# Kernel optimization log

Measured on AMD Instinct MI355X. Metric: run time of the kernel, lower is better.

## Reference

```python
import jax, jax.numpy as jnp
import numpy as np

B, GRID, DM, DEPTH = 4, 12, 384, 8
L = GRID ** 3                      # 1728 tokens
DI, NS, DC, DTR = 768, 16, 4, 24   # d_inner, d_state, d_conv, dt_rank
KEEP = 432


def _sincos_pos_embed(grid, dim):
    g = np.arange(grid, dtype=np.float32)
    gh, gw, gd = np.meshgrid(g, g, g, indexing='ij')
    pd = dim // 6
    omega = 1.0 / (10000.0 ** (np.arange(pd, dtype=np.float32) / pd))
    parts = []
    for v in (gh, gw, gd):
        o = np.einsum('m,d->md', v.reshape(-1), omega)
        parts += [np.sin(o), np.cos(o)]
    return np.concatenate(parts, axis=1)[None].astype(np.float32)  # (1, L, dim)


def setup_inputs():
    key = jax.random.key(0)
    ks = jax.random.split(key, 16)
    n = lambda k, s, sc=0.02: jax.random.normal(k, s, jnp.float32) * sc
    # mamba dt_proj bias init: inverse softplus of dt ~ LogUniform(1e-3, 1e-1)
    dt = jnp.exp(jax.random.uniform(ks[9], (DEPTH, DI)) * (np.log(0.1) - np.log(0.001)) + np.log(0.001))
    dt_proj_b = dt + jnp.log(-jnp.expm1(-dt))
    A_log = jnp.log(jnp.broadcast_to(jnp.arange(1, NS + 1, dtype=jnp.float32), (DEPTH, DI, NS)))
    rng = np.random.default_rng(0)
    act = np.zeros((B, L), np.int32)
    for b in range(B):
        act[b, rng.permutation(L)[:KEEP]] = 1
    return {
        'imgs': n(ks[0], (B, DM, GRID, GRID, GRID), 1.0),
        'pos_embed': jnp.asarray(_sincos_pos_embed(GRID, DM)),
        'mask_token': n(ks[1], (DM,)),
        'norm1_w': jnp.ones((DEPTH, DM)), 'norm1_b': jnp.zeros((DEPTH, DM)),
        'in_proj_w': n(ks[2], (DEPTH, 2 * DI, DM)),
        'conv_w': n(ks[3], (DEPTH, DI, DC), 0.1), 'conv_b': jnp.zeros((DEPTH, DI)),
        'x_proj_w': n(ks[4], (DEPTH, DTR + 2 * NS, DI)),
        'dt_proj_w': n(ks[5], (DEPTH, DI, DTR), 0.1), 'dt_proj_b': dt_proj_b,
        'A_log': A_log, 'A_b_log': A_log,
        'D_skip': jnp.ones((DEPTH, DI)),
        'out_proj_w': n(ks[6], (DEPTH, DM, DI)),
        'norm2_w': jnp.ones((DEPTH, DM)), 'norm2_b': jnp.zeros((DEPTH, DM)),
        'fc1_w': n(ks[7], (DEPTH, 2 * DM, DM)), 'fc1_b': jnp.zeros((DEPTH, 2 * DM)),
        'fc2_w': n(ks[8], (DEPTH, DM, 2 * DM)), 'fc2_b': jnp.zeros((DEPTH, DM)),
        'active': jnp.asarray(act.reshape(B, 1, GRID, GRID, GRID)),
        'len_keep': KEEP,
    }


def _ln(x, w, b):
    mu = jnp.mean(x, -1, keepdims=True)
    v = jnp.var(x, -1, keepdims=True)
    return (x - mu) * jax.lax.rsqrt(v + 1e-5) * w + b


def _ssm_dir(xr, z, conv_w, conv_b, xpw, dtw, dtb, a_log, dskip):
    # xr, z: (B, DI, Lk) pre-conv streams; causal depthwise conv then selective scan
    Lk = xr.shape[-1]
    xp = jnp.pad(xr, ((0, 0), (0, 0), (DC - 1, 0)))
    x = sum(conv_w[:, k][None, :, None] * xp[:, :, k:k + Lk] for k in range(DC))
    x = jax.nn.silu(x + conv_b[None, :, None])
    xdb = jnp.einsum('bdl,rd->brl', x, xpw)
    dtr, Bm, Cm = xdb[:, :DTR], xdb[:, DTR:DTR + NS], xdb[:, DTR + NS:]
    delta = jax.nn.softplus(jnp.einsum('brl,dr->bdl', dtr, dtw) + dtb[None, :, None])
    A = -jnp.exp(a_log)                              # (DI, NS)
    dl = delta.transpose(0, 2, 1)                    # (B, Lk, DI)
    xt = x.transpose(0, 2, 1)                        # (B, Lk, DI)
    dA = jnp.exp(dl[..., None] * A)                  # (B, Lk, DI, NS)
    dBx = dl[..., None] * Bm.transpose(0, 2, 1)[:, :, None, :] * xt[..., None]
    Ct = Cm.transpose(0, 2, 1)                       # (B, Lk, NS)

    def step(h, inp):
        a, bx, c = inp
        h = a * h + bx
        return h, jnp.einsum('bdn,bn->bd', h, c)

    h0 = jnp.zeros((xr.shape[0], DI, NS), xr.dtype)
    _, ys = jax.lax.scan(step, h0, (dA.transpose(1, 0, 2, 3), dBx.transpose(1, 0, 2, 3), Ct.transpose(1, 0, 2)))
    y = ys.transpose(1, 0, 2) + dskip * xt           # (B, Lk, DI)
    return y * jax.nn.silu(z.transpose(0, 2, 1))


def _block(x, p):
    (n1w, n1b, inW, cw, cb, xpw, dtw, dtb, al, abl, dsk, ow, n2w, n2b, f1w, f1b, f2w, f2b) = p
    h = _ln(x, n1w, n1b)
    xz = h @ inW.T                                   # (B, Lk, 2*DI)
    xr = xz[..., :DI].transpose(0, 2, 1)
    z = xz[..., DI:].transpose(0, 2, 1)
    yf = _ssm_dir(xr, z, cw, cb, xpw, dtw, dtb, al, dsk)
    yb = _ssm_dir(xr[:, :, ::-1], z[:, :, ::-1], cw, cb, xpw, dtw, dtb, abl, dsk)[:, ::-1]
    x = x + (yf + yb) @ ow.T
    h2 = _ln(x, n2w, n2b)
    return x + (jax.nn.gelu(h2 @ f1w.T + f1b, approximate=False) @ f2w.T + f2b)


def _forward(imgs, pos_embed, mask_token, norm1_w, norm1_b, in_proj_w, conv_w, conv_b,
             x_proj_w, dt_proj_w, dt_proj_b, A_log, A_b_log, D_skip, out_proj_w,
             norm2_w, norm2_b, fc1_w, fc1_b, fc2_w, fc2_b, active, len_keep):
    x = imgs.reshape(B, DM, L).transpose(0, 2, 1) + pos_embed   # (B, L, DM)
    mask = active.reshape(B, L).astype(jnp.int32)               # (B, L) 1=keep
    ids_shuffle = jnp.argsort(1 - mask, axis=1)                 # kept tokens first
    ids_restore = jnp.argsort(ids_shuffle, axis=1)
    ids_keep = ids_shuffle[:, :len_keep]
    xk = jnp.take_along_axis(x, jnp.broadcast_to(ids_keep[:, :, None], (B, len_keep, DM)), axis=1)
    blk = jax.checkpoint(_block)
    for i in range(DEPTH):
        p = (norm1_w[i], norm1_b[i], in_proj_w[i], conv_w[i], conv_b[i], x_proj_w[i],
             dt_proj_w[i], dt_proj_b[i], A_log[i], A_b_log[i], D_skip[i], out_proj_w[i],
             norm2_w[i], norm2_b[i], fc1_w[i], fc1_b[i], fc2_w[i], fc2_b[i])
        xk = blk(xk, p)
    mt = jnp.broadcast_to(mask_token, (B, L - len_keep, DM))
    x_ = jnp.concatenate([xk, mt], axis=1)
    x = jnp.take_along_axis(x_, jnp.broadcast_to(ids_restore[:, :, None], (B, L, DM)), axis=1)
    return x.transpose(0, 2, 1).reshape(B, DM, GRID, GRID, GRID)


def reference(imgs, pos_embed, mask_token, norm1_w, norm1_b, in_proj_w, conv_w, conv_b,
              x_proj_w, dt_proj_w, dt_proj_b, A_log, A_b_log, D_skip, out_proj_w,
              norm2_w, norm2_b, fc1_w, fc1_b, fc2_w, fc2_b, active, len_keep):
    return _forward(imgs, pos_embed, mask_token, norm1_w, norm1_b, in_proj_w, conv_w, conv_b,
                    x_proj_w, dt_proj_w, dt_proj_b, A_log, A_b_log, D_skip, out_proj_w,
                    norm2_w, norm2_b, fc1_w, fc1_b, fc2_w, fc2_b, active, len_keep)
```

## Files before the change

### kernel.cpp

```cpp
#include <hip/hip_runtime.h>
#include <hip/hip_bf16.h>
#include <math.h>

#define B_    4
#define GRID_ 12
#define DM_   384
#define DEPTH_ 8
#define L_    1728
#define DI_   768
#define NS_   16
#define DC_   4
#define DTR_  24
#define KEEP_ 432
#define XPR_  56
#define NC_   16
#define CL_   27
#define XSPLIT_ 4

typedef __attribute__((ext_vector_type(8))) short short8;
typedef __attribute__((ext_vector_type(4))) float floatx4;

__device__ __forceinline__ float silu_f(float x) {
    return x / (1.0f + __expf(-x));
}
__device__ __forceinline__ float softplus_f(float x) {
    return (x > 20.0f) ? x : log1pf(expf(x));
}
__device__ __forceinline__ float gelu_exact_f(float x) {
    return 0.5f * x * (1.0f + erff(x * 0.7071067811865476f));
}
__device__ __forceinline__ unsigned short f2bf(float x) {
    union { float f; unsigned int u; } c; c.f = x;
    unsigned int u = c.u;
    unsigned int r = (u + 0x7fffu + ((u >> 16) & 1u)) >> 16;
    return (unsigned short)r;
}

#define S0_ (DEPTH_ * 2 * DI_ * DM_)
#define S1_ (DEPTH_ * XPR_ * DI_)
#define S2_ (DEPTH_ * DI_ * DTR_)
#define S3_ (DEPTH_ * DM_ * DI_)
#define S4_ (DEPTH_ * 2 * DM_ * DM_)
#define S5_ (DEPTH_ * DM_ * 2 * DM_)
#define WTOT_ (S0_ + S1_ + S2_ + S3_ + S4_ + S5_)

__global__ void cast_weights_k(const float* __restrict__ w0,
                               const float* __restrict__ w1,
                               const float* __restrict__ w2,
                               const float* __restrict__ w3,
                               const float* __restrict__ w4,
                               const float* __restrict__ w5,
                               unsigned short* __restrict__ out) {
    int i = blockIdx.x * 256 + threadIdx.x;
    if (i >= WTOT_) return;
    float v;
    if (i < S0_) v = w0[i];
    else if (i < S0_ + S1_) v = w1[i - S0_];
    else if (i < S0_ + S1_ + S2_) v = w2[i - S0_ - S1_];
    else if (i < S0_ + S1_ + S2_ + S3_) v = w3[i - S0_ - S1_ - S2_];
    else if (i < S0_ + S1_ + S2_ + S3_ + S4_) v = w4[i - S0_ - S1_ - S2_ - S3_];
    else v = w5[i - S0_ - S1_ - S2_ - S3_ - S4_];
    out[i] = f2bf(v);
}

__global__ __launch_bounds__(256) void compute_ids_k(
        const int* __restrict__ active,
        int* __restrict__ RANK, int* __restrict__ IDS) {
    __shared__ int cnt[256];
    int b = blockIdx.x;
    int t = threadIdx.x;
    const int PER = (L_ + 255) / 256;
    int base = t * PER;
    int c = 0;
    for (int j = 0; j < PER; ++j) {
        int l = base + j;
        if (l < L_ && active[b * L_ + l]) ++c;
    }
    cnt[t] = c;
    __syncthreads();
    for (int off = 1; off < 256; off <<= 1) {
        int v = (t >= off) ? cnt[t - off] : 0;
        __syncthreads();
        cnt[t] += v;
        __syncthreads();
    }
    int r = cnt[t] - c;
    for (int j = 0; j < PER; ++j) {
        int l = base + j;
        if (l >= L_) break;
        if (active[b * L_ + l]) {
            RANK[b * L_ + l] = r;
            IDS[b * KEEP_ + r] = l;
            ++r;
        } else {
            RANK[b * L_ + l] = -1;
        }
    }
}

__global__ void gather_embed_k(const float* __restrict__ imgs,
                               const float* __restrict__ pos,
                               const int* __restrict__ IDS,
                               float* __restrict__ X) {
    int tid = blockIdx.x * 256 + threadIdx.x;
    if (tid >= B_ * KEEP_ * DM_) return;
    int c = tid % DM_;
    int i = (tid / DM_) % KEEP_;
    int b = tid / (DM_ * KEEP_);
    int l = IDS[b * KEEP_ + i];
    X[tid] = imgs[((size_t)b * DM_ + c) * L_ + l] + pos[(size_t)l * DM_ + c];
}

__global__ void final_scatter_k(const float* __restrict__ X,
                                const float* __restrict__ mask_token,
                                const int* __restrict__ RANK,
                                float* __restrict__ out) {
    int tid = blockIdx.x * 256 + threadIdx.x;
    if (tid >= B_ * DM_ * L_) return;
    int l = tid % L_;
    int c = (tid / L_) % DM_;
    int b = tid / (L_ * DM_);
    int r = RANK[b * L_ + l];
    out[tid] = (r >= 0) ? X[((size_t)b * KEEP_ + r) * DM_ + c] : mask_token[c];
}

__global__ void layernorm_k(const float* __restrict__ X,
                            const float* __restrict__ w,
                            const float* __restrict__ bia,
                            float* __restrict__ H, int rows) {
    int row = blockIdx.x * 4 + (threadIdx.x >> 6);
    int lane = threadIdx.x & 63;
    if (row >= rows) return;
    const float* x = X + (size_t)row * DM_;
    float v[6];
    float s = 0.0f;
#pragma unroll
    for (int j = 0; j < 6; ++j) { v[j] = x[lane + 64 * j]; s += v[j]; }
#pragma unroll
    for (int m = 1; m < 64; m <<= 1) s += __shfl_xor(s, m);
    float mu = s * (1.0f / DM_);
    float s2 = 0.0f;
#pragma unroll
    for (int j = 0; j < 6; ++j) { float d = v[j] - mu; s2 += d * d; }
#pragma unroll
    for (int m = 1; m < 64; m <<= 1) s2 += __shfl_xor(s2, m);
    float rs = rsqrtf(s2 * (1.0f / DM_) + 1e-5f);
    float* h = H + (size_t)row * DM_;
#pragma unroll
    for (int j = 0; j < 6; ++j) {
        int c = lane + 64 * j;
        h[c] = (v[j] - mu) * rs * w[c] + bia[c];
    }
}

__global__ __launch_bounds__(256) void gemm_mfma_k(
    const float* __restrict__ A, const float* __restrict__ A2, int lda,
    int aslabs, size_t aslabstride,
    const unsigned short* __restrict__ Wb,
    const float* __restrict__ bias,
    float* __restrict__ C, int ldc,
    int M, int N, int K, int kslices, int mode) {
    __shared__ unsigned short As[2][64][32];
    __shared__ unsigned short Bs[2][64][32];
    int t = threadIdx.x;
    int wave = t >> 6;
    int lane = t & 63;
    int q = lane >> 4;
    int ml = lane & 15;
    int m0 = blockIdx.y * 64;
    int n0 = blockIdx.x * 64;
    int z  = blockIdx.z;
    int Kper = K / kslices;
    int kbeg = z * Kper;
    int kend = kbeg + Kper;
    if (mode == 8) C += (size_t)z * M * ldc;

    int srow = t >> 2;
    int scol = (t & 3) * 8;

    const bool nfull = (N - n0) >= 64;

    floatx4 acc[4];
#pragma unroll
    for (int i = 0; i < 4; ++i) acc[i] = (floatx4){0.f, 0.f, 0.f, 0.f};

    float ra[8];
    uint4 rb;

    auto loadA = [&](int k0) {
        if (k0 + 32 <= kend) {
            const float* ap = A + (size_t)(m0 + srow) * lda + k0 + scol;
            floatx4 v0 = *(const floatx4*)ap;
            floatx4 v1 = *(const floatx4*)(ap + 4);
            for (int sl = 1; sl < aslabs; ++sl) {
                const float* ap2 = ap + sl * aslabstride;
                v0 += *(const floatx4*)ap2;
                v1 += *(const floatx4*)(ap2 + 4);
            }
            if (A2) {
                const float* ap2 = A2 + (size_t)(m0 + srow) * lda + k0 + scol;
                v0 += *(const floatx4*)ap2;
                v1 += *(const floatx4*)(ap2 + 4);
            }
#pragma unroll
            for (int j = 0; j < 4; ++j) { ra[j] = v0[j]; ra[4 + j] = v1[j]; }
        } else {
#pragma unroll
            for (int j = 0; j < 8; ++j) {
                int kk = k0 + scol + j;
                float v = 0.0f;
                if (kk < kend) {
                    size_t ai = (size_t)(m0 + srow) * lda + kk;
                    v = A[ai];
                    for (int sl = 1; sl < aslabs; ++sl) v += A[ai + sl * aslabstride];
                    if (A2) v += A2[ai];
                }
                ra[j] = v;
            }
        }
    };
    auto loadB = [&](int k0) {
        if (nfull && (k0 + 32 <= kend)) {
            rb = *(const uint4*)(Wb + (size_t)(n0 + srow) * K + k0 + scol);
        } else {
            unsigned short tmp[8];
#pragma unroll
            for (int j = 0; j < 8; ++j) {
                int kk = k0 + scol + j;
                unsigned short v = 0;
                if ((n0 + srow) < N && kk < kend)
                    v = Wb[(size_t)(n0 + srow) * K + kk];
                tmp[j] = v;
            }
            rb = *(const uint4*)tmp;
        }
    };
    auto storeT = [&](int buf) {
#pragma unroll
        for (int j = 0; j < 8; ++j) As[buf][srow][scol + j] = f2bf(ra[j]);
        *(uint4*)&Bs[buf][srow][scol] = rb;
    };

    int nk = (Kper + 31) >> 5;
    loadA(kbeg);
    loadB(kbeg);
    storeT(0);
    __syncthreads();
    int buf = 0;
    for (int it = 0; it < nk; ++it) {
        if (it + 1 < nk) {
            int kn = kbeg + (it + 1) * 32;
            loadA(kn);
            loadB(kn);
        }
        short8 a = *(const short8*)&As[buf][wave * 16 + ml][q * 8];
#pragma unroll
        for (int ns = 0; ns < 4; ++ns) {
            short8 b = *(const short8*)&Bs[buf][ns * 16 + ml][q * 8];
            acc[ns] = __builtin_amdgcn_mfma_f32_16x16x32_bf16(a, b, acc[ns], 0, 0, 0);
        }
        if (it + 1 < nk) {
            storeT(buf ^ 1);
            __syncthreads();
            buf ^= 1;
        }
    }

#pragma unroll
    for (int ns = 0; ns < 4; ++ns) {
        int n = n0 + ns * 16 + ml;
        if (n >= N) continue;
#pragma unroll
        for (int r = 0; r < 4; ++r) {
            int m = m0 + wave * 16 + q * 4 + r;
            float v = acc[ns][r];
            size_t ci = (size_t)m * ldc + n;
            if (mode == 2) {
                C[ci] = softplus_f(v + bias[n]);
            } else if (mode == 3) {
                C[ci] = gelu_exact_f(v + bias[n]);
            } else if (mode == 4) {
                C[ci] = v + C[ci];
            } else if (mode == 5) {
                C[ci] = v + C[ci] + bias[n];
            } else if (mode == 6) {
                atomicAdd(&C[ci], v);
            } else if (mode == 7) {
                if (z == 0) v += bias[n];
                atomicAdd(&C[ci], v);
            } else {
                C[ci] = v;
            }
        }
    }
}

__global__ void conv_silu_k(const float* __restrict__ XZ,
                            const float* __restrict__ cw,
                            const float* __restrict__ cb,
                            float* __restrict__ XCONV) {
    int tid = blockIdx.x * 256 + threadIdx.x;
    if (tid >= 2 * B_ * KEEP_ * DI_) return;
    int d = tid % DI_;
    int s = (tid / DI_) % KEEP_;
    int b = (tid / (DI_ * KEEP_)) % B_;
    int dir = tid / (DI_ * KEEP_ * B_);
    float v = cb[d];
#pragma unroll
    for (int k = 0; k < DC_; ++k) {
        int j = s - (DC_ - 1) + k;
        if (j >= 0) {
            int la = dir ? (KEEP_ - 1 - j) : j;
            v += cw[d * DC_ + k] * XZ[((size_t)b * KEEP_ + la) * (2 * DI_) + d];
        }
    }
    XCONV[tid] = silu_f(v);
}

#define PSL_ ((size_t)(2 * B_ * KEEP_) * XPR_)

__global__ __launch_bounds__(256) void scan_partial_k(
        const float* __restrict__ DELTA,
        const float* __restrict__ XCONV,
        const float* __restrict__ PART,
        const float* __restrict__ Alog,
        const float* __restrict__ Ablog,
        float* __restrict__ HFIN,
        float* __restrict__ SDELT) {
    __shared__ float sB[CL_][NS_];
    int blk = blockIdx.x;
    int g   = blk % 3;
    int c   = (blk / 3) % NC_;
    int b   = (blk / (3 * NC_)) % B_;
    int dir = blk / (3 * NC_ * B_);
    int t = threadIdx.x;
    int d = g * 256 + t;
    size_t base = (size_t)(dir * B_ + b) * KEEP_ + c * CL_;

    for (int i = t; i < CL_ * NS_; i += 256) {
        int s = i >> 4, n = i & 15;
        size_t idx = (base + s) * XPR_ + DTR_ + n;
        float v = PART[idx];
#pragma unroll
        for (int sl = 1; sl < XSPLIT_; ++sl) v += PART[idx + sl * PSL_];
        sB[s][n] = v;
    }
    __syncthreads();

    const float* alog = dir ? Ablog : Alog;
    float Av[NS_];
#pragma unroll
    for (int n = 0; n < NS_; ++n) Av[n] = -__expf(alog[d * NS_ + n]);
    float h[NS_];
#pragma unroll
    for (int n = 0; n < NS_; ++n) h[n] = 0.0f;
    float sdel = 0.0f;

    float nd = DELTA[base * DI_ + d];
    float nx = XCONV[base * DI_ + d];
    for (int s = 0; s < CL_; ++s) {
        float delta = nd, xv = nx;
        if (s + 1 < CL_) {
            nd = DELTA[(base + s + 1) * DI_ + d];
            nx = XCONV[(base + s + 1) * DI_ + d];
        }
        sdel += delta;
        float dx = delta * xv;
#pragma unroll
        for (int n = 0; n < NS_; ++n)
            h[n] = __expf(delta * Av[n]) * h[n] + dx * sB[s][n];
    }
    size_t o = ((size_t)(dir * B_ + b) * NC_ + c) * DI_ + d;
    SDELT[o] = sdel;
#pragma unroll
    for (int n = 0; n < NS_; ++n) HFIN[o * NS_ + n] = h[n];
}

__global__ __launch_bounds__(256) void scan_combine_k(
        const float* __restrict__ HFIN,
        const float* __restrict__ SDELT,
        const float* __restrict__ Alog,
        const float* __restrict__ Ablog,
        float* __restrict__ HINIT) {
    int gid = blockIdx.x * 256 + threadIdx.x;
    int n = gid & 15;
    int d = (gid >> 4) % DI_;
    int b = (gid / (16 * DI_)) % B_;
    int dir = gid / (16 * DI_ * B_);
    const float* alog = dir ? Ablog : Alog;
    float Av = -__expf(alog[d * NS_ + n]);
    float hi = 0.0f;
#pragma unroll
    for (int c = 0; c < NC_; ++c) {
        size_t o = ((size_t)(dir * B_ + b) * NC_ + c) * DI_ + d;
        HINIT[o * NS_ + n] = hi;
        hi = __expf(Av * SDELT[o]) * hi + HFIN[o * NS_ + n];
    }
}

__global__ __launch_bounds__(256) void scan_final_k(
        const float* __restrict__ DELTA,
        const float* __restrict__ XCONV,
        const float* __restrict__ PART,
        const float* __restrict__ XZ,
        const float* __restrict__ Alog,
        const float* __restrict__ Ablog,
        const float* __restrict__ dskip,
        const float* __restrict__ HINIT,
        float* __restrict__ YOUT) {
    __shared__ float sB[CL_][NS_];
    __shared__ float sC[CL_][NS_];
    int blk = blockIdx.x;
    int g   = blk % 3;
    int c   = (blk / 3) % NC_;
    int b   = (blk / (3 * NC_)) % B_;
    int dir = blk / (3 * NC_ * B_);
    int t = threadIdx.x;
    int d = g * 256 + t;
    size_t base = (size_t)(dir * B_ + b) * KEEP_ + c * CL_;

    for (int i = t; i < CL_ * NS_; i += 256) {
        int s = i >> 4, n = i & 15;
        size_t ib = (base + s) * XPR_ + DTR_ + n;
        size_t ic = ib + NS_;
        float vb = PART[ib], vc = PART[ic];
#pragma unroll
        for (int sl = 1; sl < XSPLIT_; ++sl) {
            vb += PART[ib + sl * PSL_];
            vc += PART[ic + sl * PSL_];
        }
        sB[s][n] = vb;
        sC[s][n] = vc;
    }
    __syncthreads();

    const float* alog = dir ? Ablog : Alog;
    float Av[NS_];
#pragma unroll
    for (int n = 0; n < NS_; ++n) Av[n] = -__expf(alog[d * NS_ + n]);
    float dsk = dskip[d];
    size_t o = ((size_t)(dir * B_ + b) * NC_ + c) * DI_ + d;
    float h[NS_];
#pragma unroll
    for (int n = 0; n < NS_; ++n) h[n] = HINIT[o * NS_ + n];

    float nd = DELTA[base * DI_ + d];
    float nx = XCONV[base * DI_ + d];
    for (int s = 0; s < CL_; ++s) {
        float delta = nd, xv = nx;
        if (s + 1 < CL_) {
            nd = DELTA[(base + s + 1) * DI_ + d];
            nx = XCONV[(base + s + 1) * DI_ + d];
        }
        float dx = delta * xv;
        float y = 0.0f;
#pragma unroll
        for (int n = 0; n < NS_; ++n) {
            h[n] = __expf(delta * Av[n]) * h[n] + dx * sB[s][n];
            y += h[n] * sC[s][n];
        }
        int pos = c * CL_ + s;
        int la = dir ? (KEEP_ - 1 - pos) : pos;
        float z = XZ[((size_t)b * KEEP_ + la) * (2 * DI_) + DI_ + d];
        YOUT[((size_t)(dir * B_ + b) * KEEP_ + la) * DI_ + d] =
            (y + dsk * xv) * silu_f(z);
    }
}

extern "C" void kernel_launch(void* const* d_in, const int* in_sizes, int n_in,
                              void* d_out, int out_size, void* d_ws, size_t ws_size,
                              hipStream_t stream) {
    const float* imgs      = (const float*)d_in[0];
    const float* pos       = (const float*)d_in[1];
    const float* mask_tok  = (const float*)d_in[2];
    const float* n1w       = (const float*)d_in[3];
    const float* n1b       = (const float*)d_in[4];
    const float* inW       = (const float*)d_in[5];
    const float* cw        = (const float*)d_in[6];
    const float* cb        = (const float*)d_in[7];
    const float* xpw       = (const float*)d_in[8];
    const float* dtw       = (const float*)d_in[9];
    const float* dtb       = (const float*)d_in[10];
    const float* Alog      = (const float*)d_in[11];
    const float* Ablog     = (const float*)d_in[12];
    const float* dskip     = (const float*)d_in[13];
    const float* ow        = (const float*)d_in[14];
    const float* n2w       = (const float*)d_in[15];
    const float* n2b       = (const float*)d_in[16];
    const float* f1w       = (const float*)d_in[17];
    const float* f1b       = (const float*)d_in[18];
    const float* f2w       = (const float*)d_in[19];
    const float* f2b       = (const float*)d_in[20];
    const int*   active    = (const int*)d_in[21];
    float* out = (float*)d_out;

    char* w = (char*)d_ws;
    auto alloc = [&](size_t bytes) {
        void* p = (void*)w;
        w += (bytes + 255) & ~(size_t)255;
        return p;
    };
    int*   RANK  = (int*)  alloc((size_t)B_ * L_ * 4);
    int*   IDS   = (int*)  alloc((size_t)B_ * KEEP_ * 4);
    float* X     = (float*)alloc((size_t)B_ * KEEP_ * DM_ * 4);
    float* H     = (float*)alloc((size_t)B_ * KEEP_ * DM_ * 4);
    float* XZ    = (float*)alloc((size_t)B_ * KEEP_ * 2 * DI_ * 4);
    float* XCONV = (float*)alloc((size_t)2 * B_ * KEEP_ * DI_ * 4);
    float* PART  = (float*)alloc((size_t)XSPLIT_ * 2 * B_ * KEEP_ * XPR_ * 4);
    float* DELTA = (float*)alloc((size_t)2 * B_ * KEEP_ * DI_ * 4);
    float* YOUT  = (float*)alloc((size_t)2 * B_ * KEEP_ * DI_ * 4);
    float* G     = (float*)alloc((size_t)B_ * KEEP_ * DI_ * 4);
    float* HFIN  = (float*)alloc((size_t)2 * B_ * NC_ * DI_ * NS_ * 4);
    float* HINIT = (float*)alloc((size_t)2 * B_ * NC_ * DI_ * NS_ * 4);
    float* SDELT = (float*)alloc((size_t)2 * B_ * NC_ * DI_ * 4);
    unsigned short* WB = (unsigned short*)alloc((size_t)WTOT_ * 2);

    const unsigned short* wInB = WB;
    const unsigned short* wXpB = WB + S0_;
    const unsigned short* wDtB = WB + S0_ + S1_;
    const unsigned short* wOwB = WB + S0_ + S1_ + S2_;
    const unsigned short* wF1B = WB + S0_ + S1_ + S2_ + S3_;
    const unsigned short* wF2B = WB + S0_ + S1_ + S2_ + S3_ + S4_;

    const int ROWS = B_ * KEEP_;
    const int ROWS2 = 2 * B_ * KEEP_;
    const int SCAN_BLOCKS = 2 * B_ * NC_ * 3;
    const size_t PSLAB = (size_t)ROWS2 * XPR_;

    cast_weights_k<<<(WTOT_ + 255) / 256, 256, 0, stream>>>(
        inW, xpw, dtw, ow, f1w, f2w, (unsigned short*)WB);
    compute_ids_k<<<B_, 256, 0, stream>>>(active, RANK, IDS);
    gather_embed_k<<<(B_ * KEEP_ * DM_ + 255) / 256, 256, 0, stream>>>(imgs, pos, IDS, X);

    for (int layer = 0; layer < DEPTH_; ++layer) {
        const unsigned short* L_inW = wInB + (size_t)layer * 2 * DI_ * DM_;
        const float* L_cw  = cw  + (size_t)layer * DI_ * DC_;
        const float* L_cb  = cb  + (size_t)layer * DI_;
        const unsigned short* L_xpw = wXpB + (size_t)layer * XPR_ * DI_;
        const unsigned short* L_dtw = wDtB + (size_t)layer * DI_ * DTR_;
        const float* L_dtb = dtb + (size_t)layer * DI_;
        const float* L_Al  = Alog  + (size_t)layer * DI_ * NS_;
        const float* L_Abl = Ablog + (size_t)layer * DI_ * NS_;
        const float* L_dsk = dskip + (size_t)layer * DI_;
        const unsigned short* L_ow  = wOwB + (size_t)layer * DM_ * DI_;
        const unsigned short* L_f1w = wF1B + (size_t)layer * 2 * DM_ * DM_;
        const float* L_f1b = f1b + (size_t)layer * 2 * DM_;
        const unsigned short* L_f2w = wF2B + (size_t)layer * DM_ * 2 * DM_;
        const float* L_f2b = f2b + (size_t)layer * DM_;

        layernorm_k<<<(ROWS + 3) / 4, 256, 0, stream>>>(
            X, n1w + layer * DM_, n1b + layer * DM_, H, ROWS);
        gemm_mfma_k<<<dim3((2 * DI_) / 64, ROWS / 64), 256, 0, stream>>>(
            H, nullptr, DM_, 1, 0, L_inW, nullptr, XZ, 2 * DI_,
            ROWS, 2 * DI_, DM_, 1, 0);
        conv_silu_k<<<(2 * B_ * KEEP_ * DI_ + 255) / 256, 256, 0, stream>>>(
            XZ, L_cw, L_cb, XCONV);
        gemm_mfma_k<<<dim3(1, ROWS2 / 64, XSPLIT_), 256, 0, stream>>>(
            XCONV, nullptr, DI_, 1, 0, L_xpw, nullptr, PART, XPR_,
            ROWS2, XPR_, DI_, XSPLIT_, 8);
        gemm_mfma_k<<<dim3(DI_ / 64, ROWS2 / 64), 256, 0, stream>>>(
            PART, nullptr, XPR_, XSPLIT_, PSLAB, L_dtw, L_dtb, DELTA, DI_,
            ROWS2, DI_, DTR_, 1, 2);
        scan_partial_k<<<SCAN_BLOCKS, 256, 0, stream>>>(
            DELTA, XCONV, PART, L_Al, L_Abl, HFIN, SDELT);
        scan_combine_k<<<(2 * B_ * DI_ * NS_) / 256, 256, 0, stream>>>(
            HFIN, SDELT, L_Al, L_Abl, HINIT);
        scan_final_k<<<SCAN_BLOCKS, 256, 0, stream>>>(
            DELTA, XCONV, PART, XZ, L_Al, L_Abl, L_dsk, HINIT, YOUT);
        gemm_mfma_k<<<dim3(DM_ / 64, ROWS / 64, 2), 256, 0, stream>>>(
            YOUT, YOUT + (size_t)B_ * KEEP_ * DI_, DI_, 1, 0, L_ow, nullptr,
            X, DM_, ROWS, DM_, DI_, 2, 6);
        layernorm_k<<<(ROWS + 3) / 4, 256, 0, stream>>>(
            X, n2w + layer * DM_, n2b + layer * DM_, H, ROWS);
        gemm_mfma_k<<<dim3((2 * DM_) / 64, ROWS / 64), 256, 0, stream>>>(
            H, nullptr, DM_, 1, 0, L_f1w, L_f1b, G, 2 * DM_,
            ROWS, 2 * DM_, DM_, 1, 3);
        gemm_mfma_k<<<dim3(DM_ / 64, ROWS / 64, 2), 256, 0, stream>>>(
            G, nullptr, 2 * DM_, 1, 0, L_f2w, L_f2b, X, DM_,
            ROWS, DM_, 2 * DM_, 2, 7);
    }

    final_scatter_k<<<(B_ * DM_ * L_ + 255) / 256, 256, 0, stream>>>(
        X, mask_tok, RANK, out);
}
```

Before: 1.522 ms.

## Fuse conv+dt_proj into scan and x_proj, emit bf16 activations

Fuses the depthwise conv+SiLU into the x_proj GEMM's A-load and recomputes conv and the dt_proj+softplus inside both scan kernels from XZ and the x_proj partials. This removes the XCONV and DELTA intermediates and two kernel launches per layer. LayerNorm and the fc1 GELU epilogue now write bf16, so the GEMMs load bf16 A directly. LDS tiles are padded to cut bank conflicts and the bounds-check paths are dropped. In exchange the conv and dt work is computed twice (once per scan pass), and the scan kernels use more shared memory, which may lower occupancy.

```diff
diff --git a/kernel.cpp b/kernel.cpp
--- a/kernel.cpp
+++ b/kernel.cpp
@@ -38,15 +38,13 @@
 
 #define S0_ (DEPTH_ * 2 * DI_ * DM_)
 #define S1_ (DEPTH_ * XPR_ * DI_)
-#define S2_ (DEPTH_ * DI_ * DTR_)
 #define S3_ (DEPTH_ * DM_ * DI_)
 #define S4_ (DEPTH_ * 2 * DM_ * DM_)
 #define S5_ (DEPTH_ * DM_ * 2 * DM_)
-#define WTOT_ (S0_ + S1_ + S2_ + S3_ + S4_ + S5_)
+#define WTOT_ (S0_ + S1_ + S3_ + S4_ + S5_)
 
 __global__ void cast_weights_k(const float* __restrict__ w0,
                                const float* __restrict__ w1,
-                               const float* __restrict__ w2,
                                const float* __restrict__ w3,
                                const float* __restrict__ w4,
                                const float* __restrict__ w5,
@@ -56,10 +54,9 @@
     float v;
     if (i < S0_) v = w0[i];
     else if (i < S0_ + S1_) v = w1[i - S0_];
-    else if (i < S0_ + S1_ + S2_) v = w2[i - S0_ - S1_];
-    else if (i < S0_ + S1_ + S2_ + S3_) v = w3[i - S0_ - S1_ - S2_];
-    else if (i < S0_ + S1_ + S2_ + S3_ + S4_) v = w4[i - S0_ - S1_ - S2_ - S3_];
-    else v = w5[i - S0_ - S1_ - S2_ - S3_ - S4_];
+    else if (i < S0_ + S1_ + S3_) v = w3[i - S0_ - S1_];
+    else if (i < S0_ + S1_ + S3_ + S4_) v = w4[i - S0_ - S1_ - S3_];
+    else v = w5[i - S0_ - S1_ - S3_ - S4_];
     out[i] = f2bf(v);
 }
 
@@ -127,7 +124,7 @@
 __global__ void layernorm_k(const float* __restrict__ X,
                             const float* __restrict__ w,
                             const float* __restrict__ bia,
-                            float* __restrict__ H, int rows) {
+                            unsigned short* __restrict__ H, int rows) {
     int row = blockIdx.x * 4 + (threadIdx.x >> 6);
     int lane = threadIdx.x & 63;
     if (row >= rows) return;
@@ -145,23 +142,24 @@
 #pragma unroll
     for (int m = 1; m < 64; m <<= 1) s2 += __shfl_xor(s2, m);
     float rs = rsqrtf(s2 * (1.0f / DM_) + 1e-5f);
-    float* h = H + (size_t)row * DM_;
+    unsigned short* h = H + (size_t)row * DM_;
 #pragma unroll
     for (int j = 0; j < 6; ++j) {
         int c = lane + 64 * j;
-        h[c] = (v[j] - mu) * rs * w[c] + bia[c];
-    }
-}
-
+        h[c] = f2bf((v[j] - mu) * rs * w[c] + bia[c]);
+    }
+}
+
+#define APAD_ 40
 __global__ __launch_bounds__(256) void gemm_mfma_k(
-    const float* __restrict__ A, const float* __restrict__ A2, int lda,
-    int aslabs, size_t aslabstride,
+    const void* __restrict__ Ap, const float* __restrict__ A2, int lda,
+    int abf16,
     const unsigned short* __restrict__ Wb,
     const float* __restrict__ bias,
     float* __restrict__ C, int ldc,
     int M, int N, int K, int kslices, int mode) {
-    __shared__ unsigned short As[2][64][32];
-    __shared__ unsigned short Bs[2][64][32];
+    __shared__ unsigned short As[2][64][APAD_];
+    __shared__ unsigned short Bs[2][64][APAD_];
     int t = threadIdx.x;
     int wave = t >> 6;
     int lane = t & 63;
@@ -172,31 +170,25 @@
     int z  = blockIdx.z;
     int Kper = K / kslices;
     int kbeg = z * Kper;
-    int kend = kbeg + Kper;
-    if (mode == 8) C += (size_t)z * M * ldc;
 
     int srow = t >> 2;
     int scol = (t & 3) * 8;
 
-    const bool nfull = (N - n0) >= 64;
-
     floatx4 acc[4];
 #pragma unroll
     for (int i = 0; i < 4; ++i) acc[i] = (floatx4){0.f, 0.f, 0.f, 0.f};
 
     float ra[8];
-    uint4 rb;
+    uint4 rau, rb;
 
     auto loadA = [&](int k0) {
-        if (k0 + 32 <= kend) {
-            const float* ap = A + (size_t)(m0 + srow) * lda + k0 + scol;
+        if (abf16) {
+            rau = *(const uint4*)((const unsigned short*)Ap +
+                                  (size_t)(m0 + srow) * lda + k0 + scol);
+        } else {
+            const float* ap = (const float*)Ap + (size_t)(m0 + srow) * lda + k0 + scol;
             floatx4 v0 = *(const floatx4*)ap;
             floatx4 v1 = *(const floatx4*)(ap + 4);
-            for (int sl = 1; sl < aslabs; ++sl) {
-                const float* ap2 = ap + sl * aslabstride;
-                v0 += *(const floatx4*)ap2;
-                v1 += *(const floatx4*)(ap2 + 4);
-            }
             if (A2) {
                 const float* ap2 = A2 + (size_t)(m0 + srow) * lda + k0 + scol;
                 v0 += *(const floatx4*)ap2;
@@ -204,44 +196,22 @@
             }
 #pragma unroll
             for (int j = 0; j < 4; ++j) { ra[j] = v0[j]; ra[4 + j] = v1[j]; }
-        } else {
-#pragma unroll
-            for (int j = 0; j < 8; ++j) {
-                int kk = k0 + scol + j;
-                float v = 0.0f;
-                if (kk < kend) {
-                    size_t ai = (size_t)(m0 + srow) * lda + kk;
-                    v = A[ai];
-                    for (int sl = 1; sl < aslabs; ++sl) v += A[ai + sl * aslabstride];
-                    if (A2) v += A2[ai];
-                }
-                ra[j] = v;
-            }
         }
     };
     auto loadB = [&](int k0) {
-        if (nfull && (k0 + 32 <= kend)) {
-            rb = *(const uint4*)(Wb + (size_t)(n0 + srow) * K + k0 + scol);
-        } else {
-            unsigned short tmp[8];
-#pragma unroll
-            for (int j = 0; j < 8; ++j) {
-                int kk = k0 + scol + j;
-                unsigned short v = 0;
-                if ((n0 + srow) < N && kk < kend)
-                    v = Wb[(size_t)(n0 + srow) * K + kk];
-                tmp[j] = v;
-            }
-            rb = *(const uint4*)tmp;
-        }
+        rb = *(const uint4*)(Wb + (size_t)(n0 + srow) * K + k0 + scol);
     };
     auto storeT = [&](int buf) {
-#pragma unroll
-        for (int j = 0; j < 8; ++j) As[buf][srow][scol + j] = f2bf(ra[j]);
+        if (abf16) {
+            *(uint4*)&As[buf][srow][scol] = rau;
+        } else {
+#pragma unroll
+            for (int j = 0; j < 8; ++j) As[buf][srow][scol + j] = f2bf(ra[j]);
+        }
         *(uint4*)&Bs[buf][srow][scol] = rb;
     };
 
-    int nk = (Kper + 31) >> 5;
+    int nk = Kper >> 5;
     loadA(kbeg);
     loadB(kbeg);
     storeT(0);
@@ -269,25 +239,18 @@
 #pragma unroll
     for (int ns = 0; ns < 4; ++ns) {
         int n = n0 + ns * 16 + ml;
-        if (n >= N) continue;
 #pragma unroll
         for (int r = 0; r < 4; ++r) {
             int m = m0 + wave * 16 + q * 4 + r;
             float v = acc[ns][r];
             size_t ci = (size_t)m * ldc + n;
-            if (mode == 2) {
-                C[ci] = softplus_f(v + bias[n]);
-            } else if (mode == 3) {
-                C[ci] = gelu_exact_f(v + bias[n]);
-            } else if (mode == 4) {
-                C[ci] = v + C[ci];
-            } else if (mode == 5) {
-                C[ci] = v + C[ci] + bias[n];
-            } else if (mode == 6) {
+            if (mode == 6) {
                 atomicAdd(&C[ci], v);
             } else if (mode == 7) {
                 if (z == 0) v += bias[n];
                 atomicAdd(&C[ci], v);
+            } else if (mode == 9) {
+                ((unsigned short*)C)[ci] = f2bf(gelu_exact_f(v + bias[n]));
             } else {
                 C[ci] = v;
             }
@@ -295,39 +258,137 @@
     }
 }
 
-__global__ void conv_silu_k(const float* __restrict__ XZ,
-                            const float* __restrict__ cw,
-                            const float* __restrict__ cb,
-                            float* __restrict__ XCONV) {
-    int tid = blockIdx.x * 256 + threadIdx.x;
-    if (tid >= 2 * B_ * KEEP_ * DI_) return;
-    int d = tid % DI_;
-    int s = (tid / DI_) % KEEP_;
-    int b = (tid / (DI_ * KEEP_)) % B_;
-    int dir = tid / (DI_ * KEEP_ * B_);
-    float v = cb[d];
-#pragma unroll
-    for (int k = 0; k < DC_; ++k) {
-        int j = s - (DC_ - 1) + k;
-        if (j >= 0) {
-            int la = dir ? (KEEP_ - 1 - j) : j;
-            v += cw[d * DC_ + k] * XZ[((size_t)b * KEEP_ + la) * (2 * DI_) + d];
-        }
-    }
-    XCONV[tid] = silu_f(v);
+__global__ __launch_bounds__(256) void xproj_conv_k(
+        const float* __restrict__ XZ,
+        const float* __restrict__ cw,
+        const float* __restrict__ cb,
+        const unsigned short* __restrict__ Wb,
+        float* __restrict__ Cout) {
+    __shared__ unsigned short As[2][64][APAD_];
+    __shared__ unsigned short Bs[2][64][APAD_];
+    int t = threadIdx.x;
+    int wave = t >> 6;
+    int lane = t & 63;
+    int q = lane >> 4;
+    int ml = lane & 15;
+    int m0 = blockIdx.y * 64;
+    int z  = blockIdx.z;
+    const int Kper = DI_ / XSPLIT_;
+    int kbeg = z * Kper;
+    float* C = Cout + (size_t)z * (2 * B_ * KEEP_) * XPR_;
+
+    int srow = t >> 2;
+    int scol = (t & 3) * 8;
+    int m = m0 + srow;
+    int dir = m / (B_ * KEEP_);
+    int rem = m - dir * (B_ * KEEP_);
+    int b = rem / KEEP_;
+    int s = rem - b * KEEP_;
+
+    floatx4 acc[4];
+#pragma unroll
+    for (int i = 0; i < 4; ++i) acc[i] = (floatx4){0.f, 0.f, 0.f, 0.f};
+
+    float ra[8];
+    uint4 rb;
+
+    auto loadA = [&](int k0) {
+        int d0 = k0 + scol;
+        float v[8];
+        {
+            floatx4 c0v = *(const floatx4*)(cb + d0);
+            floatx4 c1v = *(const floatx4*)(cb + d0 + 4);
+#pragma unroll
+            for (int j = 0; j < 4; ++j) { v[j] = c0v[j]; v[4 + j] = c1v[j]; }
+        }
+        float cwv[8][4];
+#pragma unroll
+        for (int jj = 0; jj < 8; ++jj) {
+            floatx4 cv = *(const floatx4*)(cw + (size_t)(d0 + jj) * 4);
+#pragma unroll
+            for (int j = 0; j < 4; ++j) cwv[jj][j] = cv[j];
+        }
+#pragma unroll
+        for (int j = 0; j < DC_; ++j) {
+            int pos = s - (DC_ - 1) + j;
+            if (pos >= 0) {
+                int la = dir ? (KEEP_ - 1 - pos) : pos;
+                const float* xp = XZ + ((size_t)b * KEEP_ + la) * (2 * DI_) + d0;
+                floatx4 x0 = *(const floatx4*)xp;
+                floatx4 x1 = *(const floatx4*)(xp + 4);
+#pragma unroll
+                for (int jj = 0; jj < 4; ++jj) v[jj] += cwv[jj][j] * x0[jj];
+#pragma unroll
+                for (int jj = 0; jj < 4; ++jj) v[4 + jj] += cwv[4 + jj][j] * x1[jj];
+            }
+        }
+#pragma unroll
+        for (int jj = 0; jj < 8; ++jj) ra[jj] = silu_f(v[jj]);
+    };
+    auto loadB = [&](int k0) {
+        if (srow < XPR_) {
+            rb = *(const uint4*)(Wb + (size_t)srow * DI_ + k0 + scol);
+        } else {
+            rb = (uint4){0u, 0u, 0u, 0u};
+        }
+    };
+    auto storeT = [&](int buf) {
+#pragma unroll
+        for (int j = 0; j < 8; ++j) As[buf][srow][scol + j] = f2bf(ra[j]);
+        *(uint4*)&Bs[buf][srow][scol] = rb;
+    };
+
+    const int nk = Kper >> 5;
+    loadA(kbeg);
+    loadB(kbeg);
+    storeT(0);
+    __syncthreads();
+    int buf = 0;
+    for (int it = 0; it < nk; ++it) {
+        if (it + 1 < nk) {
+            int kn = kbeg + (it + 1) * 32;
+            loadA(kn);
+            loadB(kn);
+        }
+        short8 a = *(const short8*)&As[buf][wave * 16 + ml][q * 8];
+#pragma unroll
+        for (int ns = 0; ns < 4; ++ns) {
+            short8 b2 = *(const short8*)&Bs[buf][ns * 16 + ml][q * 8];
+            acc[ns] = __builtin_amdgcn_mfma_f32_16x16x32_bf16(a, b2, acc[ns], 0, 0, 0);
+        }
+        if (it + 1 < nk) {
+            storeT(buf ^ 1);
+            __syncthreads();
+            buf ^= 1;
+        }
+    }
+#pragma unroll
+    for (int ns = 0; ns < 4; ++ns) {
+        int n = ns * 16 + ml;
+        if (n >= XPR_) continue;
+#pragma unroll
+        for (int r = 0; r < 4; ++r) {
+            int mm = m0 + wave * 16 + q * 4 + r;
+            C[(size_t)mm * XPR_ + n] = acc[ns][r];
+        }
+    }
 }
 
 #define PSL_ ((size_t)(2 * B_ * KEEP_) * XPR_)
 
 __global__ __launch_bounds__(256) void scan_partial_k(
-        const float* __restrict__ DELTA,
-        const float* __restrict__ XCONV,
+        const float* __restrict__ XZ,
         const float* __restrict__ PART,
+        const float* __restrict__ cw,
+        const float* __restrict__ cb,
+        const float* __restrict__ dtw,
+        const float* __restrict__ dtb,
         const float* __restrict__ Alog,
         const float* __restrict__ Ablog,
         float* __restrict__ HFIN,
         float* __restrict__ SDELT) {
-    __shared__ float sB[CL_][NS_];
+    __shared__ float sXR[CL_ + 3][256];
+    __shared__ float sXDB[CL_][XPR_];
     int blk = blockIdx.x;
     int g   = blk % 3;
     int c   = (blk / 3) % NC_;
@@ -335,40 +396,66 @@
     int dir = blk / (3 * NC_ * B_);
     int t = threadIdx.x;
     int d = g * 256 + t;
-    size_t base = (size_t)(dir * B_ + b) * KEEP_ + c * CL_;
-
-    for (int i = t; i < CL_ * NS_; i += 256) {
-        int s = i >> 4, n = i & 15;
-        size_t idx = (base + s) * XPR_ + DTR_ + n;
+    int c0 = c * CL_;
+
+    for (int r = 0; r < CL_ + 3; ++r) {
+        int pos = c0 - 3 + r;
+        float v = 0.0f;
+        if (pos >= 0) {
+            int la = dir ? (KEEP_ - 1 - pos) : pos;
+            v = XZ[((size_t)b * KEEP_ + la) * (2 * DI_) + d];
+        }
+        sXR[r][t] = v;
+    }
+    size_t rbase = ((size_t)(dir * B_ + b) * KEEP_ + c0) * XPR_;
+    for (int i = t; i < CL_ * XPR_; i += 256) {
+        size_t idx = rbase + i;
         float v = PART[idx];
 #pragma unroll
         for (int sl = 1; sl < XSPLIT_; ++sl) v += PART[idx + sl * PSL_];
-        sB[s][n] = v;
+        sXDB[i / XPR_][i % XPR_] = v;
     }
     __syncthreads();
 
+    float cwv[DC_];
+    {
+        floatx4 cv = *(const floatx4*)(cw + (size_t)d * 4);
+#pragma unroll
+        for (int j = 0; j < DC_; ++j) cwv[j] = cv[j];
+    }
+    float cbv = cb[d];
+    float dtwv[DTR_];
+#pragma unroll
+    for (int r = 0; r < DTR_ / 4; ++r) {
+        floatx4 v = *(const floatx4*)(dtw + (size_t)d * DTR_ + r * 4);
+#pragma unroll
+        for (int j = 0; j < 4; ++j) dtwv[r * 4 + j] = v[j];
+    }
+    float dtbv = dtb[d];
     const float* alog = dir ? Ablog : Alog;
     float Av[NS_];
 #pragma unroll
-    for (int n = 0; n < NS_; ++n) Av[n] = -__expf(alog[d * NS_ + n]);
+    for (int n = 0; n < NS_; ++n) Av[n] = -__expf(alog[(size_t)d * NS_ + n]);
+
     float h[NS_];
 #pragma unroll
     for (int n = 0; n < NS_; ++n) h[n] = 0.0f;
     float sdel = 0.0f;
 
-    float nd = DELTA[base * DI_ + d];
-    float nx = XCONV[base * DI_ + d];
     for (int s = 0; s < CL_; ++s) {
-        float delta = nd, xv = nx;
-        if (s + 1 < CL_) {
-            nd = DELTA[(base + s + 1) * DI_ + d];
-            nx = XCONV[(base + s + 1) * DI_ + d];
-        }
-        sdel += delta;
-        float dx = delta * xv;
+        float xv = cbv;
+#pragma unroll
+        for (int j = 0; j < DC_; ++j) xv += cwv[j] * sXR[s + j][t];
+        xv = silu_f(xv);
+        float dt = dtbv;
+#pragma unroll
+        for (int r = 0; r < DTR_; ++r) dt += dtwv[r] * sXDB[s][r];
+        dt = softplus_f(dt);
+        sdel += dt;
+        float dx = dt * xv;
 #pragma unroll
         for (int n = 0; n < NS_; ++n)
-            h[n] = __expf(delta * Av[n]) * h[n] + dx * sB[s][n];
+            h[n] = __expf(dt * Av[n]) * h[n] + dx * sXDB[s][DTR_ + n];
     }
     size_t o = ((size_t)(dir * B_ + b) * NC_ + c) * DI_ + d;
     SDELT[o] = sdel;
@@ -388,7 +475,7 @@
     int b = (gid / (16 * DI_)) % B_;
     int dir = gid / (16 * DI_ * B_);
     const float* alog = dir ? Ablog : Alog;
-    float Av = -__expf(alog[d * NS_ + n]);
+    float Av = -__expf(alog[(size_t)d * NS_ + n]);
     float hi = 0.0f;
 #pragma unroll
     for (int c = 0; c < NC_; ++c) {
@@ -399,17 +486,20 @@
 }
 
 __global__ __launch_bounds__(256) void scan_final_k(
-        const float* __restrict__ DELTA,
-        const float* __restrict__ XCONV,
+        const float* __restrict__ XZ,
         const float* __restrict__ PART,
-        const float* __restrict__ XZ,
+        const float* __restrict__ cw,
+        const float* __restrict__ cb,
+        const float* __restrict__ dtw,
+        const float* __restrict__ dtb,
         const float* __restrict__ Alog,
         const float* __restrict__ Ablog,
         const float* __restrict__ dskip,
         const float* __restrict__ HINIT,
         float* __restrict__ YOUT) {
-    __shared__ float sB[CL_][NS_];
-    __shared__ float sC[CL_][NS_];
+    __shared__ float sXR[CL_ + 3][256];
+    __shared__ float sZ[CL_][256];
+    __shared__ float sXDB[CL_][XPR_];
     int blk = blockIdx.x;
     int g   = blk % 3;
     int c   = (blk / 3) % NC_;
@@ -417,53 +507,78 @@
     int dir = blk / (3 * NC_ * B_);
     int t = threadIdx.x;
     int d = g * 256 + t;
-    size_t base = (size_t)(dir * B_ + b) * KEEP_ + c * CL_;
-
-    for (int i = t; i < CL_ * NS_; i += 256) {
-        int s = i >> 4, n = i & 15;
-        size_t ib = (base + s) * XPR_ + DTR_ + n;
-        size_t ic = ib + NS_;
-        float vb = PART[ib], vc = PART[ic];
-#pragma unroll
-        for (int sl = 1; sl < XSPLIT_; ++sl) {
-            vb += PART[ib + sl * PSL_];
-            vc += PART[ic + sl * PSL_];
-        }
-        sB[s][n] = vb;
-        sC[s][n] = vc;
+    int c0 = c * CL_;
+
+    for (int r = 0; r < CL_ + 3; ++r) {
+        int pos = c0 - 3 + r;
+        float v = 0.0f;
+        if (pos >= 0) {
+            int la = dir ? (KEEP_ - 1 - pos) : pos;
+            v = XZ[((size_t)b * KEEP_ + la) * (2 * DI_) + d];
+        }
+        sXR[r][t] = v;
+    }
+    for (int s = 0; s < CL_; ++s) {
+        int pos = c0 + s;
+        int la = dir ? (KEEP_ - 1 - pos) : pos;
+        sZ[s][t] = XZ[((size_t)b * KEEP_ + la) * (2 * DI_) + DI_ + d];
+    }
+    size_t rbase = ((size_t)(dir * B_ + b) * KEEP_ + c0) * XPR_;
+    for (int i = t; i < CL_ * XPR_; i += 256) {
+        size_t idx = rbase + i;
+        float v = PART[idx];
+#pragma unroll
+        for (int sl = 1; sl < XSPLIT_; ++sl) v += PART[idx + sl * PSL_];
+        sXDB[i / XPR_][i % XPR_] = v;
     }
     __syncthreads();
 
+    float cwv[DC_];
+    {
+        floatx4 cv = *(const floatx4*)(cw + (size_t)d * 4);
+#pragma unroll
+        for (int j = 0; j < DC_; ++j) cwv[j] = cv[j];
+    }
+    float cbv = cb[d];
+    float dtwv[DTR_];
+#pragma unroll
+    for (int r = 0; r < DTR_ / 4; ++r) {
+        floatx4 v = *(const floatx4*)(dtw + (size_t)d * DTR_ + r * 4);
+#pragma unroll
+        for (int j = 0; j < 4; ++j) dtwv[r * 4 + j] = v[j];
+    }
+    float dtbv = dtb[d];
     const float* alog = dir ? Ablog : Alog;
     float Av[NS_];
 #pragma unroll
-    for (int n = 0; n < NS_; ++n) Av[n] = -__expf(alog[d * NS_ + n]);
+    for (int n = 0; n < NS_; ++n) Av[n] = -__expf(alog[(size_t)d * NS_ + n]);
     float dsk = dskip[d];
+
     size_t o = ((size_t)(dir * B_ + b) * NC_ + c) * DI_ + d;
     float h[NS_];
 #pragma unroll
     for (int n = 0; n < NS_; ++n) h[n] = HINIT[o * NS_ + n];
 
-    float nd = DELTA[base * DI_ + d];
-    float nx = XCONV[base * DI_ + d];
     for (int s = 0; s < CL_; ++s) {
-        float delta = nd, xv = nx;
-        if (s + 1 < CL_) {
-            nd = DELTA[(base + s + 1) * DI_ + d];
-            nx = XCONV[(base + s + 1) * DI_ + d];
-        }
-        float dx = delta * xv;
+        float xv = cbv;
+#pragma unroll
+        for (int j = 0; j < DC_; ++j) xv += cwv[j] * sXR[s + j][t];
+        xv = silu_f(xv);
+        float dt = dtbv;
+#pragma unroll
+        for (int r = 0; r < DTR_; ++r) dt += dtwv[r] * sXDB[s][r];
+        dt = softplus_f(dt);
+        float dx = dt * xv;
         float y = 0.0f;
 #pragma unroll
         for (int n = 0; n < NS_; ++n) {
-            h[n] = __expf(delta * Av[n]) * h[n] + dx * sB[s][n];
-            y += h[n] * sC[s][n];
-        }
-        int pos = c * CL_ + s;
+            h[n] = __expf(dt * Av[n]) * h[n] + dx * sXDB[s][DTR_ + n];
+            y += h[n] * sXDB[s][DTR_ + NS_ + n];
+        }
+        int pos = c0 + s;
         int la = dir ? (KEEP_ - 1 - pos) : pos;
-        float z = XZ[((size_t)b * KEEP_ + la) * (2 * DI_) + DI_ + d];
         YOUT[((size_t)(dir * B_ + b) * KEEP_ + la) * DI_ + d] =
-            (y + dsk * xv) * silu_f(z);
+            (y + dsk * xv) * silu_f(sZ[s][t]);
     }
 }
 
@@ -503,13 +618,11 @@
     int*   RANK  = (int*)  alloc((size_t)B_ * L_ * 4);
     int*   IDS   = (int*)  alloc((size_t)B_ * KEEP_ * 4);
     float* X     = (float*)alloc((size_t)B_ * KEEP_ * DM_ * 4);
-    float* H     = (float*)alloc((size_t)B_ * KEEP_ * DM_ * 4);
+    unsigned short* Hb = (unsigned short*)alloc((size_t)B_ * KEEP_ * DM_ * 2);
     float* XZ    = (float*)alloc((size_t)B_ * KEEP_ * 2 * DI_ * 4);
-    float* XCONV = (float*)alloc((size_t)2 * B_ * KEEP_ * DI_ * 4);
     float* PART  = (float*)alloc((size_t)XSPLIT_ * 2 * B_ * KEEP_ * XPR_ * 4);
-    float* DELTA = (float*)alloc((size_t)2 * B_ * KEEP_ * DI_ * 4);
     float* YOUT  = (float*)alloc((size_t)2 * B_ * KEEP_ * DI_ * 4);
-    float* G     = (float*)alloc((size_t)B_ * KEEP_ * DI_ * 4);
+    unsigned short* Gb = (unsigned short*)alloc((size_t)B_ * KEEP_ * DI_ * 2);
     float* HFIN  = (float*)alloc((size_t)2 * B_ * NC_ * DI_ * NS_ * 4);
     float* HINIT = (float*)alloc((size_t)2 * B_ * NC_ * DI_ * NS_ * 4);
     float* SDELT = (float*)alloc((size_t)2 * B_ * NC_ * DI_ * 4);
@@ -517,18 +630,16 @@
 
     const unsigned short* wInB = WB;
     const unsigned short* wXpB = WB + S0_;
-    const unsigned short* wDtB = WB + S0_ + S1_;
-    const unsigned short* wOwB = WB + S0_ + S1_ + S2_;
-    const unsigned short* wF1B = WB + S0_ + S1_ + S2_ + S3_;
-    const unsigned short* wF2B = WB + S0_ + S1_ + S2_ + S3_ + S4_;
+    const unsigned short* wOwB = WB + S0_ + S1_;
+    const unsigned short* wF1B = WB + S0_ + S1_ + S3_;
+    const unsigned short* wF2B = WB + S0_ + S1_ + S3_ + S4_;
 
     const int ROWS = B_ * KEEP_;
     const int ROWS2 = 2 * B_ * KEEP_;
     const int SCAN_BLOCKS = 2 * B_ * NC_ * 3;
-    const size_t PSLAB = (size_t)ROWS2 * XPR_;
 
     cast_weights_k<<<(WTOT_ + 255) / 256, 256, 0, stream>>>(
-        inW, xpw, dtw, ow, f1w, f2w, (unsigned short*)WB);
+        inW, xpw, ow, f1w, f2w, (unsigned short*)WB);
     compute_ids_k<<<B_, 256, 0, stream>>>(active, RANK, IDS);
     gather_embed_k<<<(B_ * KEEP_ * DM_ + 255) / 256, 256, 0, stream>>>(imgs, pos, IDS, X);
 
@@ -537,7 +648,7 @@
         const float* L_cw  = cw  + (size_t)layer * DI_ * DC_;
         const float* L_cb  = cb  + (size_t)layer * DI_;
         const unsigned short* L_xpw = wXpB + (size_t)layer * XPR_ * DI_;
-        const unsigned short* L_dtw = wDtB + (size_t)layer * DI_ * DTR_;
+        const float* L_dtw = dtw + (size_t)layer * DI_ * DTR_;
         const float* L_dtb = dtb + (size_t)layer * DI_;
         const float* L_Al  = Alog  + (size_t)layer * DI_ * NS_;
         const float* L_Abl = Ablog + (size_t)layer * DI_ * NS_;
@@ -549,34 +660,28 @@
         const float* L_f2b = f2b + (size_t)layer * DM_;
 
         layernorm_k<<<(ROWS + 3) / 4, 256, 0, stream>>>(
-            X, n1w + layer * DM_, n1b + layer * DM_, H, ROWS);
+            X, n1w + layer * DM_, n1b + layer * DM_, Hb, ROWS);
         gemm_mfma_k<<<dim3((2 * DI_) / 64, ROWS / 64), 256, 0, stream>>>(
-            H, nullptr, DM_, 1, 0, L_inW, nullptr, XZ, 2 * DI_,
+            Hb, nullptr, DM_, 1, L_inW, nullptr, XZ, 2 * DI_,
             ROWS, 2 * DI_, DM_, 1, 0);
-        conv_silu_k<<<(2 * B_ * KEEP_ * DI_ + 255) / 256, 256, 0, stream>>>(
-            XZ, L_cw, L_cb, XCONV);
-        gemm_mfma_k<<<dim3(1, ROWS2 / 64, XSPLIT_), 256, 0, stream>>>(
-            XCONV, nullptr, DI_, 1, 0, L_xpw, nullptr, PART, XPR_,
-            ROWS2, XPR_, DI_, XSPLIT_, 8);
-        gemm_mfma_k<<<dim3(DI_ / 64, ROWS2 / 64), 256, 0, stream>>>(
-            PART, nullptr, XPR_, XSPLIT_, PSLAB, L_dtw, L_dtb, DELTA, DI_,
-            ROWS2, DI_, DTR_, 1, 2);
+        xproj_conv_k<<<dim3(1, ROWS2 / 64, XSPLIT_), 256, 0, stream>>>(
+            XZ, L_cw, L_cb, L_xpw, PART);
         scan_partial_k<<<SCAN_BLOCKS, 256, 0, stream>>>(
-            DELTA, XCONV, PART, L_Al, L_Abl, HFIN, SDELT);
+            XZ, PART, L_cw, L_cb, L_dtw, L_dtb, L_Al, L_Abl, HFIN, SDELT);
         scan_combine_k<<<(2 * B_ * DI_ * NS_) / 256, 256, 0, stream>>>(
             HFIN, SDELT, L_Al, L_Abl, HINIT);
         scan_final_k<<<SCAN_BLOCKS, 256, 0, stream>>>(
-            DELTA, XCONV, PART, XZ, L_Al, L_Abl, L_dsk, HINIT, YOUT);
+            XZ, PART, L_cw, L_cb, L_dtw, L_dtb, L_Al, L_Abl, L_dsk, HINIT, YOUT);
         gemm_mfma_k<<<dim3(DM_ / 64, ROWS / 64, 2), 256, 0, stream>>>(
-            YOUT, YOUT + (size_t)B_ * KEEP_ * DI_, DI_, 1, 0, L_ow, nullptr,
+            YOUT, YOUT + (size_t)B_ * KEEP_ * DI_, DI_, 0, L_ow, nullptr,
             X, DM_, ROWS, DM_, DI_, 2, 6);
         layernorm_k<<<(ROWS + 3) / 4, 256, 0, stream>>>(
-            X, n2w + layer * DM_, n2b + layer * DM_, H, ROWS);
+            X, n2w + layer * DM_, n2b + layer * DM_, Hb, ROWS);
         gemm_mfma_k<<<dim3((2 * DM_) / 64, ROWS / 64), 256, 0, stream>>>(
-            H, nullptr, DM_, 1, 0, L_f1w, L_f1b, G, 2 * DM_,
-            ROWS, 2 * DM_, DM_, 1, 3);
+            Hb, nullptr, DM_, 1, L_f1w, L_f1b, (float*)Gb, 2 * DM_,
+            ROWS, 2 * DM_, DM_, 1, 9);
         gemm_mfma_k<<<dim3(DM_ / 64, ROWS / 64, 2), 256, 0, stream>>>(
-            G, nullptr, 2 * DM_, 1, 0, L_f2w, L_f2b, X, DM_,
+            Gb, nullptr, 2 * DM_, 1, L_f2w, L_f2b, X, DM_,
             ROWS, DM_, 2 * DM_, 2, 7);
     }
 
```

Result: faster. 1.488 ms (-2.2%).
